# Kernel tuning notes

Measured on AMD Instinct MI355X. Metric: run time of the kernel, lower is better.

Reference implementation:

```python
import jax, jax.numpy as jnp
import numpy as np

B = 2048
G = 8
C = B * G  # 16384


def setup_inputs() -> dict:
    key = jax.random.key(0)
    k1, k2 = jax.random.split(key)
    student_scores = jax.random.normal(k1, (B, C), dtype=jnp.float32)
    teacher_targets = jax.random.uniform(k2, (B, G), dtype=jnp.float32)
    return {
        "student_scores": student_scores,
        "teacher_targets": teacher_targets,
        "group_size": G,
    }


def reference(student_scores, teacher_targets, group_size):
    b = student_scores.shape[0]
    rows = jnp.arange(b)
    labels = rows * group_size  # base target column per row
    neg = jnp.finfo(student_scores.dtype).min
    mask = jnp.zeros_like(student_scores)
    loss = jnp.zeros((), dtype=student_scores.dtype)
    # group_size is small and fixed (e.g. 8): Python loop over it is fine.
    for i in range(group_size):
        tgt = labels + i                       # [B]
        s = student_scores + mask              # [B, C], previously-used targets masked to -inf
        lse = jax.nn.logsumexp(s, axis=-1)     # [B]
        picked = s[rows, tgt]                  # [B] logits at the current target
        ce = lse - picked                      # per-row cross entropy, reduction='none'
        loss = loss + jnp.mean(teacher_targets[:, i] * ce)
        mask = mask.at[rows, tgt].set(neg)
    return loss
```

## Files before the change

### kernel.cpp

```cpp
#include <hip/hip_runtime.h>


#define BB 2048
#define CC 16384
#define GG 8
#define NT 256
#define NBATCH 2
#define NVEC 8

#define CNT_SHIFT 56
#define VAL_MASK ((1ull << CNT_SHIFT) - 1)
#define FIX_SCALE 268435456.0
#define LINES 32
#define LINE_STRIDE 8

typedef float f32x4 __attribute__((ext_vector_type(4)));

__global__ __launch_bounds__(NT, 8) void kd_fused_kernel(
    const float* __restrict__ scores,
    const float* __restrict__ teacher,
    unsigned long long* __restrict__ acc,
    float* __restrict__ out)
{
    const int row = blockIdx.x;
    const int tid = threadIdx.x;
    const float* rp = scores + (size_t)row * CC;
    const f32x4* rp4 = reinterpret_cast<const f32x4*>(rp);

    float t = 0.0f, w = 0.0f;
    if (tid < GG) {
        t = rp[row * GG + tid];
        w = teacher[row * GG + tid];
    }

    float s0 = 0.0f, s1 = 0.0f;
    f32x4 v[NVEC];
#pragma unroll
    for (int b = 0; b < NBATCH; ++b) {
#pragma unroll
        for (int i = 0; i < NVEC; ++i) v[i] = rp4[(b * NVEC + i) * NT + tid];
        __builtin_amdgcn_sched_barrier(0);
#pragma unroll
        for (int i = 0; i < NVEC; ++i) {
            s0 += __expf(v[i].x) + __expf(v[i].y);
            s1 += __expf(v[i].z) + __expf(v[i].w);
        }
    }
    float s = s0 + s1;

#pragma unroll
    for (int off = 32; off >= 1; off >>= 1) s += __shfl_xor(s, off);

    __shared__ float ss[NT / 64];
    const int wave = tid >> 6;
    const int lane = tid & 63;
    if (lane == 0) ss[wave] = s;
    __syncthreads();

    if (tid < GG) {
        float S = 0.0f;
#pragma unroll
        for (int q = 0; q < NT / 64; ++q) S += ss[q];

        float e = __expf(t);
        float p = e;
#pragma unroll
        for (int off = 1; off < GG; off <<= 1) {
            float o = __shfl_up(p, off, GG);
            if (tid >= off) p += o;
        }
        float S2 = S - (p - e);
        float contrib = w * (__logf(S2) - t);
#pragma unroll
        for (int off = GG / 2; off >= 1; off >>= 1)
            contrib += __shfl_xor(contrib, off, GG);

        if (tid == 0) {
            unsigned long long myv =
                (unsigned long long)((double)contrib * FIX_SCALE);
            unsigned long long pk = (1ull << CNT_SHIFT) | myv;
            unsigned long long old = atomicAdd(&acc[(row >> 6) * LINE_STRIDE], pk);
            if ((old >> CNT_SHIFT) == 63ull) {
                unsigned long long line_total = (old & VAL_MASK) + myv;
                unsigned long long gold = atomicAdd(&acc[LINES * LINE_STRIDE],
                                                    (1ull << CNT_SHIFT) | line_total);
                if ((gold >> CNT_SHIFT) == (unsigned long long)(LINES - 1)) {
                    unsigned long long total = (gold & VAL_MASK) + line_total;
                    out[0] = (float)((double)total * (1.0 / (FIX_SCALE * (double)BB)));
                }
            }
        }
    }
}

extern "C" void kernel_launch(void* const* d_in, const int* in_sizes, int n_in,
                              void* d_out, int out_size, void* d_ws, size_t ws_size,
                              hipStream_t stream) {
    const float* scores  = (const float*)d_in[0];
    const float* teacher = (const float*)d_in[1];
    unsigned long long* acc = (unsigned long long*)d_ws;
    float* out = (float*)d_out;

    hipMemsetAsync(d_ws, 0, (LINES * LINE_STRIDE + 1) * sizeof(unsigned long long),
                   stream);
    kd_fused_kernel<<<BB, NT, 0, stream>>>(scores, teacher, acc, out);
}
```

Baseline: 32.52 us.

## Replace fixed-point packed atomics with per-row partials and wrap-around counters, drop memset

```diff
diff --git a/kernel.cpp b/kernel.cpp
--- a/kernel.cpp
+++ b/kernel.cpp
@@ -8,18 +8,17 @@
 #define NBATCH 2
 #define NVEC 8
 
-#define CNT_SHIFT 56
-#define VAL_MASK ((1ull << CNT_SHIFT) - 1)
-#define FIX_SCALE 268435456.0
 #define LINES 32
-#define LINE_STRIDE 8
+#define LINE_STRIDE 16
 
 typedef float f32x4 __attribute__((ext_vector_type(4)));
 
 __global__ __launch_bounds__(NT, 8) void kd_fused_kernel(
     const float* __restrict__ scores,
     const float* __restrict__ teacher,
-    unsigned long long* __restrict__ acc,
+    float* __restrict__ partial,
+    unsigned int* __restrict__ cnt1,
+    unsigned int* __restrict__ cnt2,
     float* __restrict__ out)
 {
     const int row = blockIdx.x;
@@ -52,6 +51,7 @@
     for (int off = 32; off >= 1; off >>= 1) s += __shfl_xor(s, off);
 
     __shared__ float ss[NT / 64];
+    __shared__ int lastflag;
     const int wave = tid >> 6;
     const int lane = tid & 63;
     if (lane == 0) ss[wave] = s;
@@ -76,19 +76,38 @@
             contrib += __shfl_xor(contrib, off, GG);
 
         if (tid == 0) {
-            unsigned long long myv =
-                (unsigned long long)((double)contrib * FIX_SCALE);
-            unsigned long long pk = (1ull << CNT_SHIFT) | myv;
-            unsigned long long old = atomicAdd(&acc[(row >> 6) * LINE_STRIDE], pk);
-            if ((old >> CNT_SHIFT) == 63ull) {
-                unsigned long long line_total = (old & VAL_MASK) + myv;
-                unsigned long long gold = atomicAdd(&acc[LINES * LINE_STRIDE],
-                                                    (1ull << CNT_SHIFT) | line_total);
-                if ((gold >> CNT_SHIFT) == (unsigned long long)(LINES - 1)) {
-                    unsigned long long total = (gold & VAL_MASK) + line_total;
-                    out[0] = (float)((double)total * (1.0 / (FIX_SCALE * (double)BB)));
-                }
+            partial[row] = contrib;
+            __threadfence();
+
+            unsigned o1 = atomicAdd(&cnt1[(row >> 6) * LINE_STRIDE], 1u);
+            int done = 0;
+            if ((o1 & 63u) == 63u) {
+                unsigned o2 = atomicAdd(cnt2, 1u);
+                done = ((o2 & 31u) == 31u);
             }
+            lastflag = done;
+        }
+    }
+    __syncthreads();
+
+    if (lastflag) {
+        __threadfence();
+        float r0 = 0.0f, r1 = 0.0f;
+#pragma unroll
+        for (int j = 0; j < BB / NT; ++j) {
+            float x = partial[j * NT + tid];
+            if (j & 1) r1 += x; else r0 += x;
+        }
+        float r = r0 + r1;
+#pragma unroll
+        for (int off = 32; off >= 1; off >>= 1) r += __shfl_xor(r, off);
+        if (lane == 0) ss[wave] = r;
+        __syncthreads();
+        if (tid == 0) {
+            float R = 0.0f;
+#pragma unroll
+            for (int q = 0; q < NT / 64; ++q) R += ss[q];
+            out[0] = R * (1.0f / BB);
         }
     }
 }
@@ -98,10 +117,11 @@
                               hipStream_t stream) {
     const float* scores  = (const float*)d_in[0];
     const float* teacher = (const float*)d_in[1];
-    unsigned long long* acc = (unsigned long long*)d_ws;
+    char* ws = (char*)d_ws;
+    float* partial     = (float*)ws;
+    unsigned int* cnt1 = (unsigned int*)(ws + 8192);
+    unsigned int* cnt2 = (unsigned int*)(ws + 8192 + 2048);
     float* out = (float*)d_out;
 
-    hipMemsetAsync(d_ws, 0, (LINES * LINE_STRIDE + 1) * sizeof(unsigned long long),
-                   stream);
-    kd_fused_kernel<<<BB, NT, 0, stream>>>(scores, teacher, acc, out);
+    kd_fused_kernel<<<BB, NT, 0, stream>>>(scores, teacher, partial, cnt1, cnt2, out);
 }
```

Measured after the change: 88.58 us. 172% more time.
